# Kernel optimization log

Hardware: AMD Instinct MI355X
Metric: run time of the kernel (lower is better)

The kernel has to match this reference:

```python
import jax, jax.numpy as jnp
import numpy as np

TEMP = 0.07  # temperature used as logits / 0.07 in the original


def setup_inputs() -> dict:
    key = jax.random.key(0)
    k1, k2, k3 = jax.random.split(key, 3)
    B, N, T, L, D = 8, 128, 8, 6, 256
    meta = jax.random.normal(k1, (B, N, T, L, D), dtype=jnp.float32)
    thing = jax.random.randint(k2, (B, N, T), 0, 2, dtype=jnp.int32)
    label = jax.random.randint(k3, (B, N, T), 0, 40, dtype=jnp.int32)
    return {"meta_weight_for_con": meta, "thing_gt_idx": thing, "label_tmp": label}


def _con_loss(meta, thing, label):
    # meta: [B,N,T,L,D]; thing,label: [B,N,T]
    B, N, T, L, D = meta.shape
    P = N * T
    valid = thing.reshape(B, P).astype(bool)            # [B,P] boolean gt mask
    lab = label.reshape(B, P)                           # [B,P]
    # meta_weight_b[mask] -> [K,L,D]; permute(1,0,2) -> per-layer [K,D].
    # We keep all P positions and mask instead of compacting (jit-friendly).
    w = meta.reshape(B, P, L, D).transpose(0, 2, 1, 3)  # [B,L,P,D]
    w = w / jnp.maximum(jnp.linalg.norm(w, axis=-1, keepdims=True), 1e-12)  # F.normalize
    z = jnp.einsum('blpd,blqd->blpq', w, w) / TEMP      # similarity / temp [B,L,P,P]

    same = lab[:, :, None] == lab[:, None, :]           # [B,P,P]
    vpair = valid[:, :, None] & valid[:, None, :]
    eye = jnp.eye(P, dtype=bool)
    pos_mask = same & (~eye) & vpair                    # positives: same label, not self
    neg_mask = (~same) & vpair                          # negatives: different label

    K = valid.sum(axis=1)                               # [B] ins_num_ per batch
    pos_count = pos_mask.sum(axis=-1)                   # [B,P]
    neg_count = neg_mask.sum(axis=-1)                   # [B,P]

    # --- random positive sample per (batch, layer, row), mirroring np.random.choice ---
    u = jax.random.uniform(jax.random.key(42), (B, L, P))
    r = jnp.floor(u * pos_count[:, None, :].astype(u.dtype)).astype(jnp.int32)
    r = jnp.minimum(r, jnp.maximum(pos_count - 1, 0)[:, None, :])
    ranks = jnp.cumsum(pos_mask, axis=-1) - 1           # rank of each positive in index order
    sel = pos_mask[:, None, :, :] & (ranks[:, None, :, :] == r[..., None])  # [B,L,P,P]
    zp = jnp.sum(jnp.where(sel, z, 0.0), axis=-1)       # chosen positive logit [B,L,P]
    diag = jnp.diagonal(z, axis1=-2, axis2=-1)          # self-sim fallback when no positives
    zp = jnp.where((pos_count > 0)[:, None, :], zp, diag)

    # --- last negative (original pads by repeating the last negative to K-1) ---
    iota = jnp.arange(P)
    idx_last = jnp.max(jnp.where(neg_mask, iota[None, None, :], -1), axis=-1)  # [B,P]
    idx = jnp.broadcast_to(jnp.maximum(idx_last, 0)[:, None, :, None], (B, L, P, 1))
    zl = jnp.take_along_axis(z, idx, axis=-1)[..., 0]   # [B,L,P]

    # --- stable CE with label 0: loss = lse(logits) - zp ---
    max_n = jnp.max(jnp.where(neg_mask[:, None], z, -jnp.inf), axis=-1)  # [B,L,P]
    m = jnp.maximum(zp, max_n)
    m = jnp.where(jnp.isfinite(m), m, zp)
    sum_neg = jnp.sum(jnp.where(neg_mask[:, None], jnp.exp(z - m[..., None]), 0.0), axis=-1)
    pad = jnp.maximum((K[:, None] - 1 - neg_count), 0).astype(z.dtype)   # [B,P]
    pad_term = pad[:, None, :] * jnp.where((neg_count > 0)[:, None, :], jnp.exp(zl - m), 0.0)
    loss_row = m + jnp.log(jnp.exp(zp - m) + sum_neg + pad_term) - zp    # [B,L,P]

    row_w = valid.astype(z.dtype)
    mean_per = jnp.sum(loss_row * row_w[:, None, :], axis=-1) / jnp.maximum(K, 1)[:, None].astype(z.dtype)  # [B,L]

    gate = jnp.sum((thing.sum(axis=2) > 0), axis=1) >= 2  # skip batches with <2 gt rows
    return jnp.sum(jnp.where(gate[:, None], mean_per, 0.0))


def reference(meta_weight_for_con, thing_gt_idx, label_tmp):
    return _con_loss(meta_weight_for_con, thing_gt_idx, label_tmp)
```

## Files before the change

### kernel.cpp

```cpp
#include <hip/hip_runtime.h>
#include <stdint.h>

namespace {

constexpr int Bb = 8, Ll = 6, Dd = 256, Pp = 1024;
constexpr float SCALE_Y = 14.285714285714286f * 1.4426950408889634f;
constexpr float M0y = 21.0f;
constexpr float LN2f = 0.6931471805599453f;

typedef __attribute__((ext_vector_type(4))) float floatx4;

__device__ const int PAIRS[36] = {
  0x00,0x01,0x02,0x03,0x04,0x05,0x06,0x07,
  0x11,0x12,0x13,0x14,0x15,0x16,0x17,
  0x22,0x23,0x24,0x25,0x26,0x27,
  0x33,0x34,0x35,0x36,0x37,
  0x44,0x45,0x46,0x47,
  0x55,0x56,0x57,
  0x66,0x67,
  0x77
};

__device__ __forceinline__ void async16(const void* g, void* l) {
  __builtin_amdgcn_global_load_lds(
      (const __attribute__((address_space(1))) void*)g,
      (__attribute__((address_space(3))) void*)l, 16, 0, 0);
}

__device__ __forceinline__ uint32_t rotl32(uint32_t x, int n) {
  return (x << n) | (x >> (32 - n));
}
__device__ __forceinline__ void tf_round(uint32_t& x0, uint32_t& x1, int r) {
  x0 += x1; x1 = rotl32(x1, r); x1 ^= x0;
}
__device__ void threefry2x32(uint32_t x0, uint32_t x1, uint32_t& o0, uint32_t& o1) {
  const uint32_t k0 = 0u, k1 = 42u;
  const uint32_t k2 = k0 ^ k1 ^ 0x1BD11BDAu;
  x0 += k0; x1 += k1;
  tf_round(x0,x1,13); tf_round(x0,x1,15); tf_round(x0,x1,26); tf_round(x0,x1,6);
  x0 += k1; x1 += k2 + 1u;
  tf_round(x0,x1,17); tf_round(x0,x1,29); tf_round(x0,x1,16); tf_round(x0,x1,24);
  x0 += k2; x1 += k0 + 2u;
  tf_round(x0,x1,13); tf_round(x0,x1,15); tf_round(x0,x1,26); tf_round(x0,x1,6);
  x0 += k0; x1 += k1 + 3u;
  tf_round(x0,x1,17); tf_round(x0,x1,29); tf_round(x0,x1,16); tf_round(x0,x1,24);
  x0 += k1; x1 += k2 + 4u;
  tf_round(x0,x1,13); tf_round(x0,x1,15); tf_round(x0,x1,26); tf_round(x0,x1,6);
  x0 += k2; x1 += k0 + 5u;
  o0 = x0; o1 = x1;
}
__device__ float jax_u01(uint32_t idx) {
  const uint32_t HALF = (uint32_t)(Bb * Ll * Pp / 2);
  uint32_t o0, o1, bits;
  if (idx < HALF) { threefry2x32(idx, idx + HALF, o0, o1); bits = o0; }
  else            { threefry2x32(idx - HALF, idx, o0, o1); bits = o1; }
  return __uint_as_float((bits >> 9) | 0x3f800000u) - 1.0f;
}

__device__ __forceinline__ uint32_t fp8e4m3_rne(float x) {
  uint32_t u = __float_as_uint(x);
  const uint32_t s = (u >> 24) & 0x80u;
  u &= 0x7FFFFFFFu;
  uint32_t code;
  if (u < 0x3C800000u) {
    code = (uint32_t)__float2int_rn(__uint_as_float(u) * 512.0f);
  } else {
    const uint32_t r = (u + 0x7FFFFu + ((u >> 20) & 1u)) >> 20;
    code = r - (120u << 3);
  }
  return s | code;
}
__device__ __forceinline__ float fp8e4m3_tof(uint32_t c) {
  const uint32_t e = (c >> 3) & 15u, m = c & 7u;
  float mag;
  if (e) mag = __uint_as_float(((e + 120u) << 23) | (m << 20));
  else   mag = (float)m * 0.001953125f;
  return (c & 0x80u) ? -mag : mag;
}

__device__ __forceinline__ void fp8x4_dot(uint32_t a, uint32_t b, float& s) {
#if __has_builtin(__builtin_amdgcn_cvt_f32_fp8)
  s += __builtin_amdgcn_cvt_f32_fp8((int)a, 0) * __builtin_amdgcn_cvt_f32_fp8((int)b, 0);
  s += __builtin_amdgcn_cvt_f32_fp8((int)a, 1) * __builtin_amdgcn_cvt_f32_fp8((int)b, 1);
  s += __builtin_amdgcn_cvt_f32_fp8((int)a, 2) * __builtin_amdgcn_cvt_f32_fp8((int)b, 2);
  s += __builtin_amdgcn_cvt_f32_fp8((int)a, 3) * __builtin_amdgcn_cvt_f32_fp8((int)b, 3);
#else
  s += fp8e4m3_tof(a & 0xFF) * fp8e4m3_tof(b & 0xFF);
  s += fp8e4m3_tof((a >> 8) & 0xFF) * fp8e4m3_tof((b >> 8) & 0xFF);
  s += fp8e4m3_tof((a >> 16) & 0xFF) * fp8e4m3_tof((b >> 16) & 0xFF);
  s += fp8e4m3_tof((a >> 24) & 0xFF) * fp8e4m3_tof((b >> 24) & 0xFF);
#endif
}

constexpr int NB_ROW = Bb * Pp / 4;

__global__ void prep_k(const float* __restrict__ meta, const int* __restrict__ thing,
                       const int* __restrict__ label, uint8_t* __restrict__ wn,
                       int* __restrict__ qpos, int* __restrict__ negc,
                       int* __restrict__ qidx, int* __restrict__ Kv,
                       int* __restrict__ gatev, float* __restrict__ rowsum_g,
                       int* __restrict__ cnt2, float* __restrict__ out) {
  __shared__ int sK[256], sG[256];
  const int bid = blockIdx.x, t = threadIdx.x;

  if (bid < NB_ROW) {
    const int wid = bid * 4 + (t >> 6);
    const int lane = t & 63;
    const int b = wid >> 10, p = wid & (Pp - 1);

    const float* mbase = meta + (size_t)wid * (Ll * Dd);
    float4 v[Ll];
    #pragma unroll
    for (int k = 0; k < Ll; ++k)
      v[k] = *(const float4*)(mbase + k * Dd + lane * 4);
    float ss[Ll];
    #pragma unroll
    for (int k = 0; k < Ll; ++k)
      ss[k] = v[k].x * v[k].x + v[k].y * v[k].y + v[k].z * v[k].z + v[k].w * v[k].w;
    #pragma unroll
    for (int m = 32; m; m >>= 1) {
      #pragma unroll
      for (int k = 0; k < Ll; ++k) ss[k] += __shfl_xor(ss[k], m, 64);
    }
    #pragma unroll
    for (int k = 0; k < Ll; ++k) {
      const float inv = 1.0f / fmaxf(sqrtf(ss[k]), 1e-12f);
      uint8_t* dst = wn + ((size_t)(b * Ll + k) * Pp + p) * Dd + lane * 4;
#if __has_builtin(__builtin_amdgcn_cvt_pk_fp8_f32)
      const int lo16 = __builtin_amdgcn_cvt_pk_fp8_f32(v[k].x * inv, v[k].y * inv, 0, false);
      const uint32_t packed =
          (uint32_t)__builtin_amdgcn_cvt_pk_fp8_f32(v[k].z * inv, v[k].w * inv, lo16, true);
#else
      const uint32_t packed = fp8e4m3_rne(v[k].x * inv)
                            | (fp8e4m3_rne(v[k].y * inv) << 8)
                            | (fp8e4m3_rne(v[k].z * inv) << 16)
                            | (fp8e4m3_rne(v[k].w * inv) << 24);
#endif
      *(uint32_t*)dst = packed;
    }

    const int* lab = label + b * Pp;
    const int* th  = thing + b * Pp;
    const int myLab = lab[p];
    const bool myValid = (th[p] != 0);

    uint32_t posbits = 0;
    int cnt[16];
    int pc = 0, nc = 0, last = -1;
    #pragma unroll
    for (int c = 0; c < 16; ++c) {
      const int q = c * 64 + lane;
      const int lq = lab[q];
      const bool vq = (th[q] != 0);
      const bool same = (lq == myLab);
      const bool pos = myValid && vq && same && (q != p);
      const bool neg = myValid && vq && !same;
      uint64_t bp2 = __ballot(pos);
      uint64_t bn = __ballot(neg);
      if (pos) posbits |= (1u << c);
      cnt[c] = __popcll(bp2);
      pc += cnt[c];
      nc += __popcll(bn);
      if (bn) last = c * 64 + 63 - __clzll(bn);
    }
    int qsel[Ll];
    #pragma unroll
    for (int l = 0; l < Ll; ++l) qsel[l] = p;
    if (pc > 0) {
      for (int l = 0; l < Ll; ++l) {
        const float u = jax_u01((uint32_t)((b * Ll + l) * Pp + p));
        int r = (int)floorf(u * (float)pc);
        r = min(r, pc - 1);
        int base = 0;
        for (int c = 0; c < 16; ++c) {
          if (r < base + cnt[c]) {
            const bool mine = (posbits >> c) & 1u;
            uint64_t bm = __ballot(mine);
            uint64_t ltmask = (lane == 0) ? 0ull : (~0ull >> (64 - lane));
            int myrank = __popcll(bm & ltmask);
            bool hit = mine && (base + myrank == r);
            uint64_t hb = __ballot(hit);
            qsel[l] = c * 64 + (int)__builtin_ctzll(hb);
            break;
          }
          base += cnt[c];
        }
      }
    }
    if (lane == 0) {
      negc[wid] = nc;
      qidx[wid] = (last < 0) ? 0 : last;
      #pragma unroll
      for (int l = 0; l < Ll; ++l) qpos[(b * Ll + l) * Pp + p] = qsel[l];
    }
    return;
  }
  if (bid < NB_ROW + Bb) {
    const int b = bid - NB_ROW;
    int k = 0;
    for (int p = t; p < Pp; p += 256) k += (thing[b * Pp + p] != 0);
    int g = 0;
    if (t < 128) {
      int any = 0;
      for (int tt = 0; tt < 8; ++tt) any |= (thing[(b * 128 + t) * 8 + tt] != 0);
      g = any;
    }
    sK[t] = k; sG[t] = g;
    __syncthreads();
    for (int s = 128; s; s >>= 1) {
      if (t < s) { sK[t] += sK[t + s]; sG[t] += sG[t + s]; }
      __syncthreads();
    }
    if (t == 0) { Kv[b] = sK[0]; gatev[b] = (sG[0] >= 2) ? 1 : 0; }
    return;
  }
  if (bid < NB_ROW + Bb + 48) {
    const int zb = bid - (NB_ROW + Bb);
    const int idx = zb * 256 + t;
    *(float4*)(rowsum_g + idx * 4) = (float4){0.f, 0.f, 0.f, 0.f};
    if (zb == 0 && t < 192) { cnt2[t] = 0; cnt2[t + 192] = 0; }
    return;
  }
  if (t == 0) out[0] = 0.f;
}

__global__ __launch_bounds__(512)
void gemmfinal_k(const uint8_t* __restrict__ wn,
                 const int* __restrict__ thing, const int* __restrict__ label,
                 const int* __restrict__ qpos, const int* __restrict__ qidx,
                 const int* __restrict__ negc, const int* __restrict__ Kv,
                 const int* __restrict__ gatev, float* __restrict__ rowsum_g,
                 int* __restrict__ cnt2, float* __restrict__ out) {
  __shared__ __align__(16) uint8_t As[2 * 128 * 64];
  __shared__ __align__(16) uint8_t Bs[2 * 128 * 64];
  __shared__ int labp_s[128], valp_s[128], labq_s[128], valq_s[128];
  __shared__ float rowsum_lds[128], colsum_lds[128];
  __shared__ int fin_s[2];
  __shared__ int fin_any;
  __shared__ float sb[512];

  const int t = threadIdx.x;
  const int bid = blockIdx.x;
  const int xcd = bid & 7;
  const int chunk = bid >> 3;
  const int bl = xcd + 8 * (chunk % 6);
  const int b = bl / Ll;
  const int pair = PAIRS[chunk / 6];
  const int pt = pair >> 4, qt = pair & 15;
  const bool diag = (pt == qt);
  const int p0 = pt * 128, q0 = qt * 128;
  const int blP = bl * Pp;

  if (t == 0) fin_any = 0;
  if (t < 128) {
    labp_s[t] = label[b * Pp + p0 + t];
    valp_s[t] = thing[b * Pp + p0 + t];
    labq_s[t] = label[b * Pp + q0 + t];
    valq_s[t] = thing[b * Pp + q0 + t];
    rowsum_lds[t] = 0.f;
    colsum_lds[t] = 0.f;
  }

  const uint8_t* Wbl = wn + (size_t)bl * Pp * Dd;
  const int lane = t & 63;
  const int w = t >> 6;
  const int wr = w >> 2, wc = w & 3;
  const int cq = lane & 15, rq = lane >> 4;
  const int wbase16 = (t & ~63) * 16;

  floatx4 acc[4][2];
  #pragma unroll
  for (int i = 0; i < 4; ++i)
    #pragma unroll
    for (int j = 0; j < 2; ++j) acc[i][j] = (floatx4){0.f, 0.f, 0.f, 0.f};

  auto STAGE = [&](int bsel, int kt) {
    const int k0 = kt * 64;
    const int row = t >> 2, sp2 = t & 3;
    const int sl = sp2 ^ ((row >> 1) & 3);
    async16(Wbl + (size_t)(p0 + row) * Dd + k0 + sl * 16,
            As + bsel * 8192 + wbase16);
    if (!diag)
      async16(Wbl + (size_t)(q0 + row) * Dd + k0 + sl * 16,
              Bs + bsel * 8192 + wbase16);
  };

  STAGE(0, 0);
  __syncthreads();

  const uint8_t* Bbase0 = diag ? As : Bs;
  for (int kt = 0; kt < 4; ++kt) {
    const int bsel = kt & 1;
    if (kt < 3) STAGE(bsel ^ 1, kt + 1);
    const uint8_t* Ab = As + bsel * 8192;
    const uint8_t* Bb2 = Bbase0 + bsel * 8192;
    #pragma unroll
    for (int sub = 0; sub < 2; ++sub) {
      const int Lw = sub * 2 + (rq >> 1);
      const int off8 = (rq & 1) * 8;
      long long af[4], bfr[2];
      #pragma unroll
      for (int fi = 0; fi < 4; ++fi) {
        const int row = wr * 64 + fi * 16 + cq;
        af[fi] = *(const long long*)(Ab + row * 64 + (Lw ^ ((row >> 1) & 3)) * 16 + off8);
      }
      #pragma unroll
      for (int fj = 0; fj < 2; ++fj) {
        const int row = wc * 32 + fj * 16 + cq;
        bfr[fj] = *(const long long*)(Bb2 + row * 64 + (Lw ^ ((row >> 1) & 3)) * 16 + off8);
      }
      #pragma unroll
      for (int fi = 0; fi < 4; ++fi)
        #pragma unroll
        for (int fj = 0; fj < 2; ++fj)
          acc[fi][fj] = __builtin_amdgcn_mfma_f32_16x16x32_fp8_fp8(af[fi], bfr[fj],
                                                                   acc[fi][fj], 0, 0, 0);
    }
    __syncthreads();
  }

  int qlabv[2];
  float qvalf[2];
  float csum[2] = {0.f, 0.f};
  #pragma unroll
  for (int fj = 0; fj < 2; ++fj) {
    const int cl = wc * 32 + fj * 16 + cq;
    qlabv[fj] = labq_s[cl];
    qvalf[fj] = valq_s[cl] ? 1.f : 0.f;
  }
  #pragma unroll
  for (int fi = 0; fi < 4; ++fi) {
    #pragma unroll
    for (int reg = 0; reg < 4; ++reg) {
      const int rl = wr * 64 + fi * 16 + rq * 4 + reg;
      const int rlab = labp_s[rl];
      const float rvalf = valp_s[rl] ? 1.f : 0.f;
      float rsum = 0.f;
      #pragma unroll
      for (int fj = 0; fj < 2; ++fj) {
        const float e = exp2f(fmaf(acc[fi][fj][reg], SCALE_Y, -M0y));
        const float negm = (qlabv[fj] != rlab) ? (qvalf[fj] * rvalf) : 0.f;
        const float term = negm * e;
        rsum += term;
        csum[fj] += term;
      }
      rsum += __shfl_xor(rsum, 1); rsum += __shfl_xor(rsum, 2);
      rsum += __shfl_xor(rsum, 4); rsum += __shfl_xor(rsum, 8);
      if (cq == 0) atomicAdd(&rowsum_lds[rl], rsum);
    }
  }
  if (!diag) {
    #pragma unroll
    for (int fj = 0; fj < 2; ++fj) {
      float c = csum[fj];
      c += __shfl_xor(c, 16); c += __shfl_xor(c, 32);
      if (rq == 0) atomicAdd(&colsum_lds[wc * 32 + fj * 16 + cq], c);
    }
  }
  __syncthreads();
  if (t < 128) {
    atomicAdd(&rowsum_g[blP + p0 + t], rowsum_lds[t]);
    if (!diag) atomicAdd(&rowsum_g[blP + q0 + t], colsum_lds[t]);
  }
  __syncthreads();

  if (t == 0) {
    const int n1 = __hip_atomic_fetch_add(&cnt2[bl * 8 + pt], 1,
                                          __ATOMIC_RELAXED, __HIP_MEMORY_SCOPE_AGENT);
    fin_s[0] = (n1 == 7);
    int f1 = 0;
    if (!diag) {
      const int n2 = __hip_atomic_fetch_add(&cnt2[bl * 8 + qt], 1,
                                            __ATOMIC_RELAXED, __HIP_MEMORY_SCOPE_AGENT);
      f1 = (n2 == 7);
    }
    fin_s[1] = f1;
    if (fin_s[0] | f1) fin_any = 1;
  }
  __syncthreads();

  if (!fin_any) return;

  float accl = 0.f;
  if (gatev[b]) {
    const int Kb = Kv[b];
    const float invK = 1.f / (float)max(Kb, 1);
    const int qtr = t & 3;
    const int rrow = t >> 2;
    #pragma unroll
    for (int fr = 0; fr < 2; ++fr) {
      if (!fin_s[fr]) continue;
      const int p = (fr ? qt : pt) * 128 + rrow;
      const int valid = thing[b * Pp + p];
      const int qp = qpos[blP + p];
      const int qi = qidx[b * Pp + p];
      const uint8_t* rp = Wbl + (size_t)p  * Dd + qtr * 64;
      const uint8_t* rq2 = Wbl + (size_t)qp * Dd + qtr * 64;
      const uint8_t* rx = Wbl + (size_t)qi * Dd + qtr * 64;
      float sp = 0.f, sl = 0.f;
      #pragma unroll
      for (int i = 0; i < 4; ++i) {
        const uint4 a4 = *(const uint4*)(rp + i * 16);
        const uint4 b4 = *(const uint4*)(rq2 + i * 16);
        const uint4 c4 = *(const uint4*)(rx + i * 16);
        fp8x4_dot(a4.x, b4.x, sp); fp8x4_dot(a4.y, b4.y, sp);
        fp8x4_dot(a4.z, b4.z, sp); fp8x4_dot(a4.w, b4.w, sp);
        fp8x4_dot(a4.x, c4.x, sl); fp8x4_dot(a4.y, c4.y, sl);
        fp8x4_dot(a4.z, c4.z, sl); fp8x4_dot(a4.w, c4.w, sl);
      }
      sp += __shfl_xor(sp, 1); sp += __shfl_xor(sp, 2);
      sl += __shfl_xor(sl, 1); sl += __shfl_xor(sl, 2);
      if (qtr == 0 && valid != 0) {
        const float yp = sp * SCALE_Y, yl = sl * SCALE_Y;
        const float rs = __hip_atomic_load(&rowsum_g[blP + p],
                                           __ATOMIC_RELAXED, __HIP_MEMORY_SCOPE_AGENT);
        const int nc = negc[b * Pp + p];
        const float pad = fmaxf((float)(Kb - 1 - nc), 0.f);
        const float tot = exp2f(yp - M0y) + rs + ((nc > 0) ? pad * exp2f(yl - M0y) : 0.f);
        accl += LN2f * (M0y + log2f(tot) - yp) * invK;
      }
    }
  }
  sb[t] = accl;
  __syncthreads();
  for (int s = 256; s; s >>= 1) {
    if (t < s) sb[t] += sb[t + s];
    __syncthreads();
  }
  if (t == 0 && sb[0] != 0.f) atomicAdd(out, sb[0]);
}

}

extern "C" void kernel_launch(void* const* d_in, const int* in_sizes, int n_in,
                              void* d_out, int out_size, void* d_ws, size_t ws_size,
                              hipStream_t stream) {
  const float* meta = (const float*)d_in[0];
  const int* thing  = (const int*)d_in[1];
  const int* label  = (const int*)d_in[2];
  float* out = (float*)d_out;

  char* ws = (char*)d_ws;
  size_t off = 0;
  uint8_t* wn = (uint8_t*)(ws + off); off += (size_t)Bb * Ll * Pp * Dd;
  int* qpos  = (int*)(ws + off); off += (size_t)Bb * Ll * Pp * 4;
  int* negc  = (int*)(ws + off); off += (size_t)Bb * Pp * 4;
  int* qidx  = (int*)(ws + off); off += (size_t)Bb * Pp * 4;
  int* Kv    = (int*)(ws + off); off += 64;
  int* gatev = (int*)(ws + off); off += 64;
  float* rowsum_g = (float*)(ws + off); off += (size_t)Bb * Ll * Pp * 4;
  int* cnt2  = (int*)(ws + off); off += 384 * 4;

  const int nb_prep = NB_ROW + Bb + 48 + 1;
  prep_k<<<nb_prep, 256, 0, stream>>>(meta, thing, label, wn, qpos, negc, qidx,
                                      Kv, gatev, rowsum_g, cnt2, out);
  gemmfinal_k<<<8 * 6 * 36, 512, 0, stream>>>(wn, thing, label, qpos, qidx, negc,
                                              Kv, gatev, rowsum_g, cnt2, out);
}
```

Before: 144.1 us.

## Load GEMM fragments directly from global memory instead of LDS staging

Removes the double-buffered async global-to-LDS staging of the FP8 normalized weight tiles. MFMA operand fragments are now loaded straight from global memory, 8 bytes per lane per k-step, using precomputed row pointers. This drops LDS usage, the per-step barriers and the swizzle arithmetic. In exchange each wave now issues many small, partly uncoalesced global loads and repeats loads that other waves also make, so it relies on L1/L2 hits and has no explicit prefetch.

```diff
diff --git a/kernel.cpp b/kernel.cpp
--- a/kernel.cpp
+++ b/kernel.cpp
@@ -20,12 +20,6 @@
   0x66,0x67,
   0x77
 };
-
-__device__ __forceinline__ void async16(const void* g, void* l) {
-  __builtin_amdgcn_global_load_lds(
-      (const __attribute__((address_space(1))) void*)g,
-      (__attribute__((address_space(3))) void*)l, 16, 0, 0);
-}
 
 __device__ __forceinline__ uint32_t rotl32(uint32_t x, int n) {
   return (x << n) | (x >> (32 - n));
@@ -231,8 +225,6 @@
                  const int* __restrict__ negc, const int* __restrict__ Kv,
                  const int* __restrict__ gatev, float* __restrict__ rowsum_g,
                  int* __restrict__ cnt2, float* __restrict__ out) {
-  __shared__ __align__(16) uint8_t As[2 * 128 * 64];
-  __shared__ __align__(16) uint8_t Bs[2 * 128 * 64];
   __shared__ int labp_s[128], valp_s[128], labq_s[128], valq_s[128];
   __shared__ float rowsum_lds[128], colsum_lds[128];
   __shared__ int fin_s[2];
@@ -266,7 +258,16 @@
   const int w = t >> 6;
   const int wr = w >> 2, wc = w & 3;
   const int cq = lane & 15, rq = lane >> 4;
-  const int wbase16 = (t & ~63) * 16;
+
+  const int coff = (rq >> 1) * 16 + (rq & 1) * 8;
+  const uint8_t* arow[4];
+  const uint8_t* brow[2];
+  #pragma unroll
+  for (int fi = 0; fi < 4; ++fi)
+    arow[fi] = Wbl + (size_t)(p0 + wr * 64 + fi * 16 + cq) * Dd + coff;
+  #pragma unroll
+  for (int fj = 0; fj < 2; ++fj)
+    brow[fj] = Wbl + (size_t)(q0 + wc * 32 + fj * 16 + cq) * Dd + coff;
 
   floatx4 acc[4][2];
   #pragma unroll
@@ -274,50 +275,24 @@
     #pragma unroll
     for (int j = 0; j < 2; ++j) acc[i][j] = (floatx4){0.f, 0.f, 0.f, 0.f};
 
-  auto STAGE = [&](int bsel, int kt) {
-    const int k0 = kt * 64;
-    const int row = t >> 2, sp2 = t & 3;
-    const int sl = sp2 ^ ((row >> 1) & 3);
-    async16(Wbl + (size_t)(p0 + row) * Dd + k0 + sl * 16,
-            As + bsel * 8192 + wbase16);
-    if (!diag)
-      async16(Wbl + (size_t)(q0 + row) * Dd + k0 + sl * 16,
-              Bs + bsel * 8192 + wbase16);
-  };
-
-  STAGE(0, 0);
+  #pragma unroll
+  for (int sub = 0; sub < 8; ++sub) {
+    long long af[4], bfr[2];
+    #pragma unroll
+    for (int fi = 0; fi < 4; ++fi)
+      af[fi] = *(const long long*)(arow[fi] + sub * 32);
+    #pragma unroll
+    for (int fj = 0; fj < 2; ++fj)
+      bfr[fj] = *(const long long*)(brow[fj] + sub * 32);
+    #pragma unroll
+    for (int fi = 0; fi < 4; ++fi)
+      #pragma unroll
+      for (int fj = 0; fj < 2; ++fj)
+        acc[fi][fj] = __builtin_amdgcn_mfma_f32_16x16x32_fp8_fp8(af[fi], bfr[fj],
+                                                                 acc[fi][fj], 0, 0, 0);
+  }
+
   __syncthreads();
-
-  const uint8_t* Bbase0 = diag ? As : Bs;
-  for (int kt = 0; kt < 4; ++kt) {
-    const int bsel = kt & 1;
-    if (kt < 3) STAGE(bsel ^ 1, kt + 1);
-    const uint8_t* Ab = As + bsel * 8192;
-    const uint8_t* Bb2 = Bbase0 + bsel * 8192;
-    #pragma unroll
-    for (int sub = 0; sub < 2; ++sub) {
-      const int Lw = sub * 2 + (rq >> 1);
-      const int off8 = (rq & 1) * 8;
-      long long af[4], bfr[2];
-      #pragma unroll
-      for (int fi = 0; fi < 4; ++fi) {
-        const int row = wr * 64 + fi * 16 + cq;
-        af[fi] = *(const long long*)(Ab + row * 64 + (Lw ^ ((row >> 1) & 3)) * 16 + off8);
-      }
-      #pragma unroll
-      for (int fj = 0; fj < 2; ++fj) {
-        const int row = wc * 32 + fj * 16 + cq;
-        bfr[fj] = *(const long long*)(Bb2 + row * 64 + (Lw ^ ((row >> 1) & 3)) * 16 + off8);
-      }
-      #pragma unroll
-      for (int fi = 0; fi < 4; ++fi)
-        #pragma unroll
-        for (int fj = 0; fj < 2; ++fj)
-          acc[fi][fj] = __builtin_amdgcn_mfma_f32_16x16x32_fp8_fp8(af[fi], bfr[fj],
-                                                                   acc[fi][fj], 0, 0, 0);
-    }
-    __syncthreads();
-  }
 
   int qlabv[2];
   float qvalf[2];
```

After: 186.5 us. 29.4% more time.
